# Optimization experiments

Hardware: AMD Instinct MI355X
Metric: run time of the kernel (lower is better)

Reference implementation:

```python
import jax, jax.numpy as jnp
import numpy as np

C = 512
GROUPS = 8
EPS = 1e-5


def setup_inputs() -> dict:
    key = jax.random.key(0)
    ks = jax.random.split(key, 7)
    B, H, W = 16, 32, 32
    x = jax.random.normal(ks[0], (B, C, H, W), dtype=jnp.float32)
    gn_w = jnp.ones((C,), jnp.float32)
    gn_b = jnp.zeros((C,), jnp.float32)
    s = 1.0 / np.sqrt(C)
    qkv_w = jax.random.normal(ks[1], (3 * C, C), dtype=jnp.float32) * s
    qkv_b = jnp.zeros((3 * C,), jnp.float32)
    proj_w = jax.random.normal(ks[2], (C, C), dtype=jnp.float32) * s
    proj_b = jnp.zeros((C,), jnp.float32)
    return {"x": x, "gn_w": gn_w, "gn_b": gn_b, "qkv_w": qkv_w,
            "qkv_b": qkv_b, "proj_w": proj_w, "proj_b": proj_b}


def _group_norm(x, w, b):
    B, Cc, H, W = x.shape
    xg = x.reshape(B, GROUPS, Cc // GROUPS, H, W)
    mean = xg.mean(axis=(2, 3, 4), keepdims=True)
    var = xg.var(axis=(2, 3, 4), keepdims=True)
    xn = ((xg - mean) * jax.lax.rsqrt(var + EPS)).reshape(B, Cc, H, W)
    return xn * w[None, :, None, None] + b[None, :, None, None]


def reference(x, gn_w, gn_b, qkv_w, qkv_b, proj_w, proj_b):
    B, Cc, H, W = x.shape
    N = H * W
    h = _group_norm(x, gn_w, gn_b)
    # 1x1 conv == per-pixel matmul over channels
    qkv = jnp.einsum('bchw,oc->bohw', h, qkv_w) + qkv_b[None, :, None, None]
    q, k, v = jnp.split(qkv, 3, axis=1)          # each (B, C, H, W)
    q = q.reshape(B, Cc, N).transpose(0, 2, 1)   # (B, N, C)
    k = k.reshape(B, Cc, N)                      # (B, C, N)
    v = v.reshape(B, Cc, N).transpose(0, 2, 1)   # (B, N, C)
    attn = jnp.einsum('bnc,bcm->bnm', q, k) * (Cc ** -0.5)
    attn = jax.nn.softmax(attn, axis=-1)
    h = jnp.einsum('bnm,bmc->bnc', attn, v)      # (B, N, C)
    h = h.transpose(0, 2, 1).reshape(B, Cc, H, W)
    out = jnp.einsum('bchw,oc->bohw', h, proj_w) + proj_b[None, :, None, None]
    return x + out
```

## Files before the change

kernel.cpp:

```cpp
#include <hip/hip_runtime.h>


typedef __bf16 bf16x8 __attribute__((ext_vector_type(8)));
typedef float f32x4 __attribute__((ext_vector_type(4)));
typedef unsigned short u16x8 __attribute__((ext_vector_type(8)));
typedef unsigned short u16x4 __attribute__((ext_vector_type(4)));

#define DEVINL __device__ __forceinline__

DEVINL float b2f(unsigned short u) {
  unsigned int x = ((unsigned int)u) << 16;
  return __builtin_bit_cast(float, x);
}
DEVINL unsigned short f2b(float f) {
  unsigned int x = __builtin_bit_cast(unsigned int, f);
  x += 0x7fffu + ((x >> 16) & 1u);
  return (unsigned short)(x >> 16);
}

DEVINL void gload16(const void* g, void* l) {
  __builtin_amdgcn_global_load_lds(
      (const __attribute__((address_space(1))) unsigned int*)(const void*)g,
      (__attribute__((address_space(3))) unsigned int*)l, 16, 0, 0);
}

__global__ __launch_bounds__(256)
void f2bf_k(const float* __restrict__ in, unsigned short* __restrict__ out, int n4) {
  int i = blockIdx.x * 256 + threadIdx.x;
  if (i < n4) {
    float4 v = ((const float4*)in)[i];
    u16x4 o;
    o[0] = f2b(v.x); o[1] = f2b(v.y); o[2] = f2b(v.z); o[3] = f2b(v.w);
    ((u16x4*)out)[i] = o;
  }
}

__global__ __launch_bounds__(256)
void gn_stats(const float* __restrict__ x, float* __restrict__ mean, float* __restrict__ rstd) {
  const int g = blockIdx.x;
  const float4* p = (const float4*)(x + (long long)g * 65536);
  float s = 0.f, q = 0.f;
  for (int i = threadIdx.x; i < 16384; i += 256) {
    float4 v = p[i];
    s += v.x + v.y + v.z + v.w;
    q += v.x * v.x + v.y * v.y + v.z * v.z + v.w * v.w;
  }
#pragma unroll
  for (int off = 32; off; off >>= 1) { s += __shfl_xor(s, off); q += __shfl_xor(q, off); }
  __shared__ float ss[4], qs[4];
  const int wave = threadIdx.x >> 6, lane = threadIdx.x & 63;
  if (lane == 0) { ss[wave] = s; qs[wave] = q; }
  __syncthreads();
  if (threadIdx.x == 0) {
    float S = ss[0] + ss[1] + ss[2] + ss[3];
    float Q = qs[0] + qs[1] + qs[2] + qs[3];
    float mu = S * (1.f / 65536.f);
    float var = Q * (1.f / 65536.f) - mu * mu;
    mean[g] = mu;
    rstd[g] = rsqrtf(var + 1e-5f);
  }
}

__global__ __launch_bounds__(256)
void gn_apply_t(const float* __restrict__ x, const float* __restrict__ mean,
                const float* __restrict__ rstd, const float* __restrict__ gw,
                const float* __restrict__ gb, unsigned short* __restrict__ h) {
  const int b = blockIdx.z, ct = blockIdx.y, pt = blockIdx.x;
  const int c0 = ct << 6, p0 = pt << 6;
  const float mu = mean[b * 8 + ct];
  const float rs = rstd[b * 8 + ct];
  __shared__ float t[64][65];
  const int r4 = threadIdx.x >> 6, cl = threadIdx.x & 63;
#pragma unroll
  for (int i = 0; i < 16; ++i) {
    int r = i * 4 + r4;
    int c = c0 + r;
    float v = x[(long long)(b * 512 + c) * 1024 + p0 + cl];
    t[r][cl] = (v - mu) * rs * gw[c] + gb[c];
  }
  __syncthreads();
#pragma unroll
  for (int i = 0; i < 16; ++i) {
    int pr = i * 4 + r4;
    h[(long long)(b * 1024 + p0 + pr) * 512 + c0 + cl] = f2b(t[cl][pr]);
  }
}

__global__ __launch_bounds__(256)
void vtrans(const unsigned short* __restrict__ qkv, unsigned short* __restrict__ vt) {
  const int b = blockIdx.z, ct = blockIdx.y, pt = blockIdx.x;
  const int c0 = ct << 6, p0 = pt << 6;
  const unsigned short* src = qkv + (long long)b * 1024 * 1536 + 1024;
  unsigned short* dst = vt + (long long)b * 512 * 1024;
  __shared__ unsigned short t[64][65];
  const int r4 = threadIdx.x >> 6, cl = threadIdx.x & 63;
#pragma unroll
  for (int i = 0; i < 16; ++i) {
    int pr = i * 4 + r4;
    t[pr][cl] = src[(long long)(p0 + pr) * 1536 + c0 + cl];
  }
  __syncthreads();
#pragma unroll
  for (int i = 0; i < 16; ++i) {
    int cr = i * 4 + r4;
    dst[(long long)(c0 + cr) * 1024 + p0 + cl] = t[cl][cr];
  }
}

__global__ __launch_bounds__(256)
void softmax_rows(unsigned short* __restrict__ S) {
  const long long row = (long long)blockIdx.x * 4 + (threadIdx.x >> 6);
  const int lane = threadIdx.x & 63;
  u16x8* p = (u16x8*)(S + row * 1024);
  u16x8 a = p[lane], b = p[64 + lane];
  float v[16];
#pragma unroll
  for (int i = 0; i < 8; ++i) { v[i] = b2f(a[i]); v[8 + i] = b2f(b[i]); }
  float m = v[0];
#pragma unroll
  for (int i = 1; i < 16; ++i) m = fmaxf(m, v[i]);
#pragma unroll
  for (int off = 32; off; off >>= 1) m = fmaxf(m, __shfl_xor(m, off));
  float s = 0.f;
#pragma unroll
  for (int i = 0; i < 16; ++i) { v[i] = __expf(v[i] - m); s += v[i]; }
#pragma unroll
  for (int off = 32; off; off >>= 1) s += __shfl_xor(s, off);
  float inv = 1.f / s;
#pragma unroll
  for (int i = 0; i < 8; ++i) { a[i] = f2b(v[i] * inv); b[i] = f2b(v[8 + i] * inv); }
  p[lane] = a;
  p[64 + lane] = b;
}

#define RSQRT_C 0.044194173824159216f
enum { EPI_BF16 = 0, EPI_QKV = 1, EPI_PROJ = 2 };

DEVINL void stage_tile(const unsigned short* __restrict__ Ab,
                       const unsigned short* __restrict__ Bb,
                       int lda, int ldb, int k0, char* lb, int tid, int wave) {
#pragma unroll
  for (int i = 0; i < 4; ++i) {
    const int c = (i << 8) + tid;
    const int r = c >> 3;
    const int sk = ((c & 7) ^ (r & 7)) << 3;
    char* la = lb + (((i << 8) + (wave << 6)) << 4);
    gload16(Ab + (long long)r * lda + k0 + sk, la);
    gload16(Bb + (long long)r * ldb + k0 + sk, la + 16384);
  }
}

template <int EPI>
__global__ __launch_bounds__(256, 2)
void gemm_bt(const unsigned short* __restrict__ A, int lda, long long sA,
             const unsigned short* __restrict__ B, int ldb, long long sB,
             void* __restrict__ Cv, int ldc, long long sC, int K,
             const float* __restrict__ bias, const float* __restrict__ resid,
             int gx, int gy) {
  __shared__ char lds[65536];
  const int tid = threadIdx.x;
  const int wave = tid >> 6, lane = tid & 63;
  const int wr = wave >> 1, wc = wave & 1;

  const int nwg = gridDim.x;
  const int id0 = blockIdx.x;
  const int id = (id0 & 7) * (nwg >> 3) + (id0 >> 3);
  const int bn = id % gx;
  const int t1 = id / gx;
  const int bm = t1 % gy;
  const int bz = t1 / gy;

  const unsigned short* Ab = A + (long long)bz * sA + (long long)bm * 128 * lda;
  const unsigned short* Bb = B + (long long)bz * sB + (long long)bn * 128 * ldb;

  f32x4 acc[4][4] = {};
  const int frow = lane & 15;
  const int fkb = (lane >> 4) << 4;
  const int swr = (frow & 7) << 4;
  const int NT = K >> 6;

  stage_tile(Ab, Bb, lda, ldb, 0, lds, tid, wave);
  stage_tile(Ab, Bb, lda, ldb, 64, lds + 32768, tid, wave);
  asm volatile("s_waitcnt vmcnt(8)" ::: "memory");

  for (int kt = 0; kt < NT; ++kt) {
    const int cur = kt & 1;
    __builtin_amdgcn_s_barrier();
    asm volatile("" ::: "memory");
    const char* lb = lds + cur * 32768;
    __builtin_amdgcn_s_setprio(1);
#pragma unroll
    for (int ks = 0; ks < 2; ++ks) {
      bf16x8 af[4], bfr[4];
      const int kb = (ks << 6) + fkb;
#pragma unroll
      for (int f = 0; f < 4; ++f) {
        const int ar = (wr << 6) + (f << 4) + frow;
        af[f] = *reinterpret_cast<const bf16x8*>(lb + ar * 128 + (kb ^ swr));
        const int br = (wc << 6) + (f << 4) + frow;
        bfr[f] = *reinterpret_cast<const bf16x8*>(lb + 16384 + br * 128 + (kb ^ swr));
      }
#pragma unroll
      for (int i = 0; i < 4; ++i)
#pragma unroll
        for (int j = 0; j < 4; ++j)
          acc[i][j] = __builtin_amdgcn_mfma_f32_16x16x32_bf16(af[i], bfr[j], acc[i][j], 0, 0, 0);
    }
    __builtin_amdgcn_s_setprio(0);
    asm volatile("" ::: "memory");
    __builtin_amdgcn_s_barrier();
    if (kt + 2 < NT) {
      stage_tile(Ab, Bb, lda, ldb, (kt + 2) << 6, lds + cur * 32768, tid, wave);
      asm volatile("s_waitcnt vmcnt(8)" ::: "memory");
    } else if (kt + 2 == NT) {
      asm volatile("s_waitcnt vmcnt(0)" ::: "memory");
    }
  }

  const int rb = bm * 128 + (wr << 6) + ((lane >> 4) << 2);
  const int cb = bn * 128 + (wc << 6) + (lane & 15);
#pragma unroll
  for (int i = 0; i < 4; ++i) {
#pragma unroll
    for (int j = 0; j < 4; ++j) {
      const int col = cb + (j << 4);
#pragma unroll
      for (int r = 0; r < 4; ++r) {
        const int row = rb + (i << 4) + r;
        float v = acc[i][j][r];
        if constexpr (EPI == EPI_BF16) {
          ((unsigned short*)Cv)[(long long)bz * sC + (long long)row * ldc + col] = f2b(v);
        } else if constexpr (EPI == EPI_QKV) {
          v += bias[col];
          if (col < 512) v *= RSQRT_C;
          ((unsigned short*)Cv)[(long long)bz * sC + (long long)row * ldc + col] = f2b(v);
        } else {
          long long idx = (long long)bz * sC + (long long)row * ldc + col;
          ((float*)Cv)[idx] = v + bias[row] + resid[idx];
        }
      }
    }
  }
}

extern "C" void kernel_launch(void* const* d_in, const int* in_sizes, int n_in,
                              void* d_out, int out_size, void* d_ws, size_t ws_size,
                              hipStream_t stream) {
  const float* x      = (const float*)d_in[0];
  const float* gn_w   = (const float*)d_in[1];
  const float* gn_b   = (const float*)d_in[2];
  const float* qkv_w  = (const float*)d_in[3];
  const float* qkv_b  = (const float*)d_in[4];
  const float* proj_w = (const float*)d_in[5];
  const float* proj_b = (const float*)d_in[6];

  char* ws = (char*)d_ws;
  float* mean          = (float*)(ws + 0);
  float* rstd          = (float*)(ws + 512);
  unsigned short* wq   = (unsigned short*)(ws + 1024);
  unsigned short* wp   = (unsigned short*)(ws + 1573888);
  unsigned short* h    = (unsigned short*)(ws + 2098176);
  unsigned short* qkv  = (unsigned short*)(ws + 18875392);
  unsigned short* vt   = h;
  unsigned short* O    = qkv;
  unsigned short* S    = (unsigned short*)d_out;

  f2bf_k<<<768, 256, 0, stream>>>(qkv_w, wq, 196608);
  f2bf_k<<<256, 256, 0, stream>>>(proj_w, wp, 65536);
  gn_stats<<<128, 256, 0, stream>>>(x, mean, rstd);
  gn_apply_t<<<dim3(16, 8, 16), 256, 0, stream>>>(x, mean, rstd, gn_w, gn_b, h);
  gemm_bt<EPI_QKV><<<1536, 256, 0, stream>>>(
      h, 512, 0, wq, 512, 0, qkv, 1536, 0, 512, qkv_b, nullptr, 12, 128);
  gemm_bt<EPI_BF16><<<1024, 256, 0, stream>>>(
      qkv, 1536, 1024LL * 1536, qkv + 512, 1536, 1024LL * 1536,
      S, 1024, 1024LL * 1024, 512, nullptr, nullptr, 8, 8);
  softmax_rows<<<4096, 256, 0, stream>>>(S);
  vtrans<<<dim3(16, 8, 16), 256, 0, stream>>>(qkv, vt);
  gemm_bt<EPI_BF16><<<512, 256, 0, stream>>>(
      S, 1024, 1024LL * 1024, vt, 1024, 512LL * 1024,
      O, 512, 1024LL * 512, 1024, nullptr, nullptr, 4, 8);
  gemm_bt<EPI_PROJ><<<512, 256, 0, stream>>>(
      wp, 512, 0, O, 512, 1024LL * 512,
      d_out, 1024, 512LL * 1024, 512, proj_b, x, 8, 4);
}
```

Measured before the change: 243.8 us.

## Fuse group-norm passes, merge weight casts, write transposed V from QKV epilogue

```diff
diff --git a/kernel.cpp b/kernel.cpp
--- a/kernel.cpp
+++ b/kernel.cpp
@@ -25,85 +25,62 @@
 }
 
 __global__ __launch_bounds__(256)
-void f2bf_k(const float* __restrict__ in, unsigned short* __restrict__ out, int n4) {
-  int i = blockIdx.x * 256 + threadIdx.x;
-  if (i < n4) {
-    float4 v = ((const float4*)in)[i];
-    u16x4 o;
-    o[0] = f2b(v.x); o[1] = f2b(v.y); o[2] = f2b(v.z); o[3] = f2b(v.w);
-    ((u16x4*)out)[i] = o;
-  }
-}
-
-__global__ __launch_bounds__(256)
-void gn_stats(const float* __restrict__ x, float* __restrict__ mean, float* __restrict__ rstd) {
-  const int g = blockIdx.x;
-  const float4* p = (const float4*)(x + (long long)g * 65536);
+void f2bf_all(const float* __restrict__ qw, const float* __restrict__ pw,
+              unsigned short* __restrict__ wq, unsigned short* __restrict__ wp) {
+  const int i = blockIdx.x * 256 + threadIdx.x;
+  const bool isq = i < 196608;
+  const int j = isq ? i : i - 196608;
+  float4 v = isq ? ((const float4*)qw)[j] : ((const float4*)pw)[j];
+  u16x4 o;
+  o[0] = f2b(v.x); o[1] = f2b(v.y); o[2] = f2b(v.z); o[3] = f2b(v.w);
+  if (isq) ((u16x4*)wq)[j] = o; else ((u16x4*)wp)[j] = o;
+}
+
+__global__ __launch_bounds__(512)
+void gn_fused(const float* __restrict__ x, const float* __restrict__ gw,
+              const float* __restrict__ gb, unsigned short* __restrict__ h) {
+  const int b = blockIdx.x >> 3, g = blockIdx.x & 7;
+  const float* base = x + (long long)(b * 512 + g * 64) * 1024;
   float s = 0.f, q = 0.f;
-  for (int i = threadIdx.x; i < 16384; i += 256) {
-    float4 v = p[i];
+  for (int i = threadIdx.x; i < 16384; i += 512) {
+    float4 v = ((const float4*)base)[i];
     s += v.x + v.y + v.z + v.w;
     q += v.x * v.x + v.y * v.y + v.z * v.z + v.w * v.w;
   }
 #pragma unroll
   for (int off = 32; off; off >>= 1) { s += __shfl_xor(s, off); q += __shfl_xor(q, off); }
-  __shared__ float ss[4], qs[4];
+  __shared__ float ss[8], qs[8], stats[2];
   const int wave = threadIdx.x >> 6, lane = threadIdx.x & 63;
   if (lane == 0) { ss[wave] = s; qs[wave] = q; }
   __syncthreads();
   if (threadIdx.x == 0) {
-    float S = ss[0] + ss[1] + ss[2] + ss[3];
-    float Q = qs[0] + qs[1] + qs[2] + qs[3];
+    float S = 0.f, Q = 0.f;
+#pragma unroll
+    for (int w = 0; w < 8; ++w) { S += ss[w]; Q += qs[w]; }
     float mu = S * (1.f / 65536.f);
     float var = Q * (1.f / 65536.f) - mu * mu;
-    mean[g] = mu;
-    rstd[g] = rsqrtf(var + 1e-5f);
-  }
-}
-
-__global__ __launch_bounds__(256)
-void gn_apply_t(const float* __restrict__ x, const float* __restrict__ mean,
-                const float* __restrict__ rstd, const float* __restrict__ gw,
-                const float* __restrict__ gb, unsigned short* __restrict__ h) {
-  const int b = blockIdx.z, ct = blockIdx.y, pt = blockIdx.x;
-  const int c0 = ct << 6, p0 = pt << 6;
-  const float mu = mean[b * 8 + ct];
-  const float rs = rstd[b * 8 + ct];
+    stats[0] = mu;
+    stats[1] = rsqrtf(var + 1e-5f);
+  }
+  __syncthreads();
+  const float mu = stats[0], rs = stats[1];
   __shared__ float t[64][65];
-  const int r4 = threadIdx.x >> 6, cl = threadIdx.x & 63;
-#pragma unroll
-  for (int i = 0; i < 16; ++i) {
-    int r = i * 4 + r4;
-    int c = c0 + r;
-    float v = x[(long long)(b * 512 + c) * 1024 + p0 + cl];
-    t[r][cl] = (v - mu) * rs * gw[c] + gb[c];
-  }
-  __syncthreads();
-#pragma unroll
-  for (int i = 0; i < 16; ++i) {
-    int pr = i * 4 + r4;
-    h[(long long)(b * 1024 + p0 + pr) * 512 + c0 + cl] = f2b(t[cl][pr]);
-  }
-}
-
-__global__ __launch_bounds__(256)
-void vtrans(const unsigned short* __restrict__ qkv, unsigned short* __restrict__ vt) {
-  const int b = blockIdx.z, ct = blockIdx.y, pt = blockIdx.x;
-  const int c0 = ct << 6, p0 = pt << 6;
-  const unsigned short* src = qkv + (long long)b * 1024 * 1536 + 1024;
-  unsigned short* dst = vt + (long long)b * 512 * 1024;
-  __shared__ unsigned short t[64][65];
-  const int r4 = threadIdx.x >> 6, cl = threadIdx.x & 63;
-#pragma unroll
-  for (int i = 0; i < 16; ++i) {
-    int pr = i * 4 + r4;
-    t[pr][cl] = src[(long long)(p0 + pr) * 1536 + c0 + cl];
-  }
-  __syncthreads();
-#pragma unroll
-  for (int i = 0; i < 16; ++i) {
-    int cr = i * 4 + r4;
-    dst[(long long)(c0 + cr) * 1024 + p0 + cl] = t[cl][cr];
+  const int r8 = threadIdx.x >> 6, cl = threadIdx.x & 63;
+  for (int pt = 0; pt < 16; ++pt) {
+    const int p0 = pt << 6;
+#pragma unroll
+    for (int i = 0; i < 8; ++i) {
+      int c = i * 8 + r8;
+      float v = base[(long long)c * 1024 + p0 + cl];
+      t[c][cl] = (v - mu) * rs * gw[g * 64 + c] + gb[g * 64 + c];
+    }
+    __syncthreads();
+#pragma unroll
+    for (int i = 0; i < 8; ++i) {
+      int pr = i * 8 + r8;
+      h[(long long)(b * 1024 + p0 + pr) * 512 + g * 64 + cl] = f2b(t[cl][pr]);
+    }
+    __syncthreads();
   }
 }
 
@@ -156,7 +133,7 @@
              const unsigned short* __restrict__ B, int ldb, long long sB,
              void* __restrict__ Cv, int ldc, long long sC, int K,
              const float* __restrict__ bias, const float* __restrict__ resid,
-             int gx, int gy) {
+             unsigned short* __restrict__ aux, int gx, int gy) {
   __shared__ char lds[65536];
   const int tid = threadIdx.x;
   const int wave = tid >> 6, lane = tid & 63;
@@ -224,6 +201,17 @@
 #pragma unroll
     for (int j = 0; j < 4; ++j) {
       const int col = cb + (j << 4);
+      if constexpr (EPI == EPI_QKV) {
+        if (col >= 1024) {
+          const int row0 = rb + (i << 4);
+          const int bb = row0 >> 10, p0 = row0 & 1023;
+          u16x4 o;
+#pragma unroll
+          for (int r = 0; r < 4; ++r) o[r] = f2b(acc[i][j][r] + bias[col]);
+          *(u16x4*)(aux + (long long)bb * 524288 + (long long)(col - 1024) * 1024 + p0) = o;
+          continue;
+        }
+      }
 #pragma unroll
       for (int r = 0; r < 4; ++r) {
         const int row = rb + (i << 4) + r;
@@ -233,7 +221,7 @@
         } else if constexpr (EPI == EPI_QKV) {
           v += bias[col];
           if (col < 512) v *= RSQRT_C;
-          ((unsigned short*)Cv)[(long long)bz * sC + (long long)row * ldc + col] = f2b(v);
+          ((unsigned short*)Cv)[(long long)row * ldc + col] = f2b(v);
         } else {
           long long idx = (long long)bz * sC + (long long)row * ldc + col;
           ((float*)Cv)[idx] = v + bias[row] + resid[idx];
@@ -255,31 +243,26 @@
   const float* proj_b = (const float*)d_in[6];
 
   char* ws = (char*)d_ws;
-  float* mean          = (float*)(ws + 0);
-  float* rstd          = (float*)(ws + 512);
   unsigned short* wq   = (unsigned short*)(ws + 1024);
   unsigned short* wp   = (unsigned short*)(ws + 1573888);
   unsigned short* h    = (unsigned short*)(ws + 2098176);
   unsigned short* qkv  = (unsigned short*)(ws + 18875392);
-  unsigned short* vt   = h;
-  unsigned short* O    = qkv;
+  unsigned short* vt   = (unsigned short*)(ws + 52429824);
+  unsigned short* O    = h;
   unsigned short* S    = (unsigned short*)d_out;
 
-  f2bf_k<<<768, 256, 0, stream>>>(qkv_w, wq, 196608);
-  f2bf_k<<<256, 256, 0, stream>>>(proj_w, wp, 65536);
-  gn_stats<<<128, 256, 0, stream>>>(x, mean, rstd);
-  gn_apply_t<<<dim3(16, 8, 16), 256, 0, stream>>>(x, mean, rstd, gn_w, gn_b, h);
+  f2bf_all<<<1024, 256, 0, stream>>>(qkv_w, proj_w, wq, wp);
+  gn_fused<<<128, 512, 0, stream>>>(x, gn_w, gn_b, h);
   gemm_bt<EPI_QKV><<<1536, 256, 0, stream>>>(
-      h, 512, 0, wq, 512, 0, qkv, 1536, 0, 512, qkv_b, nullptr, 12, 128);
+      h, 512, 0, wq, 512, 0, qkv, 1024, 0, 512, qkv_b, nullptr, vt, 12, 128);
   gemm_bt<EPI_BF16><<<1024, 256, 0, stream>>>(
-      qkv, 1536, 1024LL * 1536, qkv + 512, 1536, 1024LL * 1536,
-      S, 1024, 1024LL * 1024, 512, nullptr, nullptr, 8, 8);
+      qkv, 1024, 1024LL * 1024, qkv + 512, 1024, 1024LL * 1024,
+      S, 1024, 1024LL * 1024, 512, nullptr, nullptr, nullptr, 8, 8);
   softmax_rows<<<4096, 256, 0, stream>>>(S);
-  vtrans<<<dim3(16, 8, 16), 256, 0, stream>>>(qkv, vt);
   gemm_bt<EPI_BF16><<<512, 256, 0, stream>>>(
       S, 1024, 1024LL * 1024, vt, 1024, 512LL * 1024,
-      O, 512, 1024LL * 512, 1024, nullptr, nullptr, 4, 8);
+      O, 512, 1024LL * 512, 1024, nullptr, nullptr, nullptr, 4, 8);
   gemm_bt<EPI_PROJ><<<512, 256, 0, stream>>>(
       wp, 512, 0, O, 512, 1024LL * 512,
-      d_out, 1024, 512LL * 1024, 512, proj_b, x, 8, 4);
-}
+      d_out, 1024, 512LL * 1024, 512, proj_b, x, nullptr, 8, 4);
+}
```

Measured after the change: 237.5 us. 1.03x faster.
